# Optimization experiments

Measured on AMD Instinct MI355X. Metric: run time of the kernel, lower is better.

Reference implementation:

```python
import jax, jax.numpy as jnp
import numpy as np

N_NODES = 20000
OUT_DEG = 16
E = N_NODES * OUT_DEG          # 320000 directed edges
F = 20                          # edge_features
H3 = 3 * F


def _lin(key, fan_in, fan_out):
    kw, kb = jax.random.split(key)
    bound = 1.0 / np.sqrt(fan_in)
    W = jax.random.uniform(kw, (fan_in, fan_out), jnp.float32, -bound, bound)
    b = jax.random.uniform(kb, (fan_out,), jnp.float32, -bound, bound)
    return W, b


def setup_inputs() -> dict:
    key = jax.random.key(0)
    rng = np.random.default_rng(0)
    # graph: every node has exactly OUT_DEG out-edges, no self-loops
    src = np.repeat(np.arange(N_NODES, dtype=np.int64), OUT_DEG)
    dst = (src + 1 + rng.integers(0, N_NODES - 1, size=E)) % N_NODES
    edge_index = jnp.asarray(np.stack([src, dst]), dtype=jnp.int32)
    # edge adjacency per _build_edge_adj: edge i=(u->v) pairs with each out-edge j of v.
    # Edges are grouped by src, so out-edges of node v are [v*OUT_DEG, v*OUT_DEG+OUT_DEG).
    # No self-loops => i != j always, so exactly E*OUT_DEG pairs.
    adj_src = jnp.asarray(np.repeat(np.arange(E, dtype=np.int64), OUT_DEG).astype(np.int32))
    adj_nbr = jnp.asarray((dst[:, None] * OUT_DEG + np.arange(OUT_DEG)).reshape(-1).astype(np.int32))

    ks = jax.random.split(key, 8)
    edge_attr = jax.random.normal(ks[0], (E, F), jnp.float32)
    msg_W1, msg_b1 = _lin(ks[1], 2 * F, 32)
    msg_W2, msg_b2 = _lin(ks[2], 32, F)
    # torch GRUCell params: weight_ih/hh are [3H, H]
    bound = 1.0 / np.sqrt(F)
    g = jax.random.split(ks[3], 4)
    gru_Wih = jax.random.uniform(g[0], (H3, F), jnp.float32, -bound, bound)
    gru_Whh = jax.random.uniform(g[1], (H3, F), jnp.float32, -bound, bound)
    gru_bih = jax.random.uniform(g[2], (H3,), jnp.float32, -bound, bound)
    gru_bhh = jax.random.uniform(g[3], (H3,), jnp.float32, -bound, bound)
    ro_W1, ro_b1 = _lin(ks[4], F, 64)
    ro_W2, ro_b2 = _lin(ks[5], 64, 32)
    ro_W3, ro_b3 = _lin(ks[6], 32, 1)
    return {
        'edge_attr': edge_attr,
        'msg_W1': msg_W1, 'msg_b1': msg_b1, 'msg_W2': msg_W2, 'msg_b2': msg_b2,
        'gru_Wih': gru_Wih, 'gru_Whh': gru_Whh, 'gru_bih': gru_bih, 'gru_bhh': gru_bhh,
        'ro_W1': ro_W1, 'ro_b1': ro_b1, 'ro_W2': ro_W2, 'ro_b2': ro_b2,
        'ro_W3': ro_W3, 'ro_b3': ro_b3,
        'edge_index': edge_index, 'adj_src': adj_src, 'adj_nbr': adj_nbr,
    }


def reference(edge_attr, msg_W1, msg_b1, msg_W2, msg_b2,
              gru_Wih, gru_Whh, gru_bih, gru_bhh,
              ro_W1, ro_b1, ro_W2, ro_b2, ro_W3, ro_b3,
              edge_index, adj_src, adj_nbr):
    num_e = edge_attr.shape[0]

    def step(h, _):
        h_i = h[adj_src]                       # [P, F] gather
        h_j = h[adj_nbr]                       # [P, F] gather
        m = jnp.concatenate([h_i, h_j], axis=-1)  # [P, 2F]
        m = jax.nn.selu(m @ msg_W1 + msg_b1) @ msg_W2 + msg_b2  # [P, F]
        agg = jax.ops.segment_sum(m, adj_src, num_segments=num_e)  # scatter_add
        # torch.nn.GRUCell(agg, h)
        gi = agg @ gru_Wih.T + gru_bih
        gh = h @ gru_Whh.T + gru_bhh
        i_r, i_z, i_n = jnp.split(gi, 3, axis=-1)
        h_r, h_z, h_n = jnp.split(gh, 3, axis=-1)
        r = jax.nn.sigmoid(i_r + h_r)
        z = jax.nn.sigmoid(i_z + h_z)
        n = jnp.tanh(i_n + r * h_n)
        return (1.0 - z) * n + z * h, None

    h_t, _ = jax.lax.scan(step, edge_attr, None, length=4)
    h_base = h_t[:num_e]  # num_edges == E here
    x = jax.nn.selu(h_base @ ro_W1 + ro_b1)
    x = jax.nn.selu(x @ ro_W2 + ro_b2)
    w = jax.nn.softplus(x @ ro_W3 + ro_b3).squeeze(-1) + 0.1
    return jnp.clip(w, 0.1, 10.0)
```

## Files before the change

### kernel.cpp

```cpp
#include <hip/hip_runtime.h>
#include <hip/hip_fp16.h>

#define E_EDGES 320000
#define NF 20

typedef float v4 __attribute__((ext_vector_type(4)));
typedef float v2f __attribute__((ext_vector_type(2)));

#if defined(__has_builtin)
# if __has_builtin(__builtin_elementwise_fma)
#  define EWFMA(a,b,c) __builtin_elementwise_fma((a),(b),(c))
# endif
#endif
#ifndef EWFMA
# define EWFMA(a,b,c) ((a)*(b)+(c))
#endif
#if defined(__has_builtin)
# if __has_builtin(__builtin_elementwise_max)
#  define EWMAX(a,b) __builtin_elementwise_max((a),(b))
#  define EWMIN(a,b) __builtin_elementwise_min((a),(b))
# endif
#endif

#if defined(__has_builtin)
# if __has_builtin(__builtin_amdgcn_exp2f)
#  define EX2F(x) __builtin_amdgcn_exp2f(x)
# endif
#endif
#ifndef EX2F
# define EX2F(x) exp2f(x)
#endif

#define LOG2E_F 1.4426950408889634f
#define SELU_SCALE 1.0507009873554805f
#define SELU_ALPHA 1.6732632423543772f
#define SELU_KA (SELU_SCALE * SELU_ALPHA)
#define SELU_SC2 (SELU_SCALE / LOG2E_F)

__device__ __forceinline__ v4 bc4(float s) { return (v4){s, s, s, s}; }
__device__ __forceinline__ v4 v4z() { return (v4){0.f, 0.f, 0.f, 0.f}; }

#define DPP_XOR1 0xB1
#define DPP_XOR2 0x4E
template<int CTRL>
__device__ __forceinline__ float dppf(float x) {
    return __builtin_bit_cast(float,
        __builtin_amdgcn_update_dpp(0, __builtin_bit_cast(int, x), CTRL, 0xF, 0xF, true));
}
template<int CTRL>
__device__ __forceinline__ v4 dpp4(v4 x) {
    v4 r;
    r.x = dppf<CTRL>(x.x); r.y = dppf<CTRL>(x.y);
    r.z = dppf<CTRL>(x.z); r.w = dppf<CTRL>(x.w);
    return r;
}

__device__ __forceinline__ float selu_f(float x) {
    const float scale = SELU_SCALE;
    const float alpha = SELU_ALPHA;
    float p = fmaxf(x, 0.f);
    float m = fminf(x, 0.f);
    float e = __expf(m);
    return fmaf(scale, p, scale * alpha * (e - 1.f));
}
__device__ __forceinline__ float sigmoid_f(float x) {
    return 1.f / (1.f + __expf(-x));
}
__device__ __forceinline__ v4 selu4(v4 x) {
    const float scale = SELU_SCALE;
    const float ka = SELU_KA;
#ifdef EWMAX
    v4 p = EWMAX(x, v4z());
    v4 m = EWMIN(x, v4z());
#else
    v4 p = {fmaxf(x.x,0.f), fmaxf(x.y,0.f), fmaxf(x.z,0.f), fmaxf(x.w,0.f)};
    v4 m = {fminf(x.x,0.f), fminf(x.y,0.f), fminf(x.z,0.f), fminf(x.w,0.f)};
#endif
    v4 e = {__expf(m.x), __expf(m.y), __expf(m.z), __expf(m.w)};
    return EWFMA(bc4(scale), p, EWFMA(bc4(ka), e, bc4(-ka)));
}

__device__ __forceinline__ float hsum4(v4 x) {
    v2f lo = __builtin_shufflevector(x, x, 0, 1);
    v2f hi = __builtin_shufflevector(x, x, 2, 3);
    v2f h = lo + hi;
    return h.x + h.y;
}

__device__ __forceinline__ float dot20v(v4 a0, v4 a1, v4 a2, v4 a3, v4 a4,
                                        const v4* __restrict__ w) {
    v4 w0 = w[0], w1 = w[1], w2 = w[2], w3 = w[3], w4 = w[4];
    v4 x = a0 * w0;
    x = EWFMA(a1, w1, x); x = EWFMA(a2, w2, x);
    x = EWFMA(a3, w3, x); x = EWFMA(a4, w4, x);
    return hsum4(x);
}
__device__ __forceinline__ void dot20_dualv(const v4* __restrict__ w,
    v4 a0, v4 a1, v4 a2, v4 a3, v4 a4,
    v4 b0, v4 b1, v4 b2, v4 b3, v4 b4,
    float& r0, float& r1)
{
    v4 w0 = w[0], w1 = w[1], w2 = w[2], w3 = w[3], w4 = w[4];
    v4 xa = a0 * w0;
    xa = EWFMA(a1, w1, xa); xa = EWFMA(a2, w2, xa);
    xa = EWFMA(a3, w3, xa); xa = EWFMA(a4, w4, xa);
    v4 xb = b0 * w0;
    xb = EWFMA(b1, w1, xb); xb = EWFMA(b2, w2, xb);
    xb = EWFMA(b3, w3, xb); xb = EWFMA(b4, w4, xb);
    r0 = hsum4(xa);
    r1 = hsum4(xb);
}
__device__ __forceinline__ void h8_to_v4x2(uint4 r, v4& lo, v4& hi) {
    float2 fa = __half22float2(__builtin_bit_cast(__half2, r.x));
    float2 fb = __half22float2(__builtin_bit_cast(__half2, r.y));
    float2 fc = __half22float2(__builtin_bit_cast(__half2, r.z));
    float2 fd = __half22float2(__builtin_bit_cast(__half2, r.w));
    lo = (v4){fa.x, fa.y, fb.x, fb.y};
    hi = (v4){fc.x, fc.y, fd.x, fd.y};
}
__device__ __forceinline__ uint4 f8_to_h8(v4 lo, v4 hi) {
    uint4 r;
    r.x = __builtin_bit_cast(unsigned, __floats2half2_rn(lo.x, lo.y));
    r.y = __builtin_bit_cast(unsigned, __floats2half2_rn(lo.z, lo.w));
    r.z = __builtin_bit_cast(unsigned, __floats2half2_rn(hi.x, hi.y));
    r.w = __builtin_bit_cast(unsigned, __floats2half2_rn(hi.z, hi.w));
    return r;
}

#define FOR20(X) \
  X(0, v0.x) X(1, v0.y) X(2, v0.z) X(3, v0.w) \
  X(4, v1.x) X(5, v1.y) X(6, v1.z) X(7, v1.w) \
  X(8, v2.x) X(9, v2.y) X(10, v2.z) X(11, v2.w) \
  X(12, v3.x) X(13, v3.y) X(14, v3.z) X(15, v3.w) \
  X(16, v4v.x) X(17, v4v.y) X(18, v4v.z) X(19, v4v.w)

#define FOR20_2(X) \
  X(0, va0.x, vb0.x) X(1, va0.y, vb0.y) X(2, va0.z, vb0.z) X(3, va0.w, vb0.w) \
  X(4, va1.x, vb1.x) X(5, va1.y, vb1.y) X(6, va1.z, vb1.z) X(7, va1.w, vb1.w) \
  X(8, va2.x, vb2.x) X(9, va2.y, vb2.y) X(10, va2.z, vb2.z) X(11, va2.w, vb2.w) \
  X(12, va3.x, vb3.x) X(13, va3.y, vb3.y) X(14, va3.z, vb3.z) X(15, va3.w, vb3.w) \
  X(16, va4.x, vb4.x) X(17, va4.y, vb4.y) X(18, va4.z, vb4.z) X(19, va4.w, vb4.w)

#define FOR8S2(X) \
  X(0, sa0.x, sb0.x) X(1, sa0.y, sb0.y) X(2, sa0.z, sb0.z) X(3, sa0.w, sb0.w) \
  X(4, sa1.x, sb1.x) X(5, sa1.y, sb1.y) X(6, sa1.z, sb1.z) X(7, sa1.w, sb1.w)

__global__ void __launch_bounds__(256) kernel_B0(
    const float* __restrict__ h, const float* __restrict__ W1,
    const float* __restrict__ b1, __half* __restrict__ B)
{
    __shared__ __align__(16) float sw[640];
    __shared__ __align__(16) float sbias[32];
    for (int i = threadIdx.x; i < 640; i += 256) sw[i] = W1[640 + i] * LOG2E_F;
    if (threadIdx.x < 32) sbias[threadIdx.x] = b1[threadIdx.x] * LOG2E_F;
    __syncthreads();
    int e = blockIdx.x * 256 + threadIdx.x;
    const v4* hp = reinterpret_cast<const v4*>(h + (size_t)e * NF);
    v4 v0 = hp[0], v1 = hp[1], v2 = hp[2], v3 = hp[3], v4v = hp[4];
    const v4* bi = reinterpret_cast<const v4*>(sbias);
    v4 c0 = bi[0], c1 = bi[1], c2 = bi[2], c3 = bi[3],
       c4 = bi[4], c5 = bi[5], c6 = bi[6], c7 = bi[7];
    #define BSTEP(f, hf) { v4 t_ = bc4(hf); const v4* w_ = (const v4*)&sw[(f)*32]; \
        c0 = EWFMA(t_, w_[0], c0); c1 = EWFMA(t_, w_[1], c1); \
        c2 = EWFMA(t_, w_[2], c2); c3 = EWFMA(t_, w_[3], c3); \
        c4 = EWFMA(t_, w_[4], c4); c5 = EWFMA(t_, w_[5], c5); \
        c6 = EWFMA(t_, w_[6], c6); c7 = EWFMA(t_, w_[7], c7); }
    FOR20(BSTEP)
    #undef BSTEP
    uint4* Bp = reinterpret_cast<uint4*>(B + (size_t)e * 32);
    Bp[0] = f8_to_h8(c0, c1); Bp[1] = f8_to_h8(c2, c3);
    Bp[2] = f8_to_h8(c4, c5); Bp[3] = f8_to_h8(c6, c7);
}

template<bool WRITEB>
__global__ void __launch_bounds__(256) kernel_stepT(
    const float* __restrict__ h_in, float* __restrict__ h_out,
    const __half* __restrict__ Br, const int* __restrict__ dst,
    const float* __restrict__ W1, const float* __restrict__ b1,
    const float* __restrict__ W2, const float* __restrict__ b2,
    const float* __restrict__ Wih, const float* __restrict__ Whh,
    const float* __restrict__ bih, const float* __restrict__ bhh,
    __half* __restrict__ Bw)
{
    __shared__ __align__(16) float sW1[640];
    __shared__ __align__(16) float sW1h[640];
    __shared__ __align__(16) float sb1h[32];
    __shared__ __align__(16) float sW2[640];
    __shared__ __align__(16) float sb2v[20];
    __shared__ __align__(16) float sCorr[20];
    __shared__ __align__(16) float sWih[1200];
    __shared__ __align__(16) float sWhh[1200];
    __shared__ float sbih[60];
    __shared__ float sbhh[60];
    for (int i = threadIdx.x; i < 640; i += 256) {
        sW1[i] = W1[i] * LOG2E_F;
        sW2[i] = W2[i];
        if (WRITEB) sW1h[i] = W1[640 + i] * LOG2E_F;
    }
    for (int i = threadIdx.x; i < 1200; i += 256) { sWih[i] = Wih[i]; sWhh[i] = Whh[i]; }
    if (threadIdx.x < 20) sb2v[threadIdx.x] = b2[threadIdx.x];
    else if (threadIdx.x >= 64 && threadIdx.x < 124) sbih[threadIdx.x - 64] = bih[threadIdx.x - 64];
    else if (threadIdx.x >= 128 && threadIdx.x < 188) sbhh[threadIdx.x - 128] = bhh[threadIdx.x - 128];
    else if (WRITEB && threadIdx.x >= 192 && threadIdx.x < 224)
        sb1h[threadIdx.x - 192] = b1[threadIdx.x - 192] * LOG2E_F;
    __syncthreads();
    if (threadIdx.x < 20) {
        float s = 0.f;
        #pragma unroll
        for (int o = 0; o < 32; o++) s += sW2[o * 20 + threadIdx.x];
        sCorr[threadIdx.x] = 16.f * (sb2v[threadIdx.x] - SELU_KA * s);
    }
    __syncthreads();

    int t = blockIdx.x * 256 + threadIdx.x;
    int p = t >> 2;
    int q = t & 3;
    int ob = q * 8;
    int e0 = p * 2, e1 = p * 2 + 1;

    int2 dd = *reinterpret_cast<const int2*>(dst + e0);
    int d0 = dd.x, d1 = dd.y;

    const v4* hp0 = reinterpret_cast<const v4*>(h_in + (size_t)e0 * NF);
    const v4* hp1 = reinterpret_cast<const v4*>(h_in + (size_t)e1 * NF);
    v4 va0 = hp0[0], va1 = hp0[1], va2 = hp0[2], va3 = hp0[3], va4 = hp0[4];
    v4 vb0 = hp1[0], vb1 = hp1[1], vb2 = hp1[2], vb3 = hp1[3], vb4 = hp1[4];

    v4 aa0 = v4z(), aa1 = v4z(), ab0 = v4z(), ab1 = v4z();
    #define ASTEP2(f, h0, h1) { const v4* w_ = (const v4*)&sW1[(f)*32 + ob]; \
        v4 w0_ = w_[0], w1_ = w_[1]; \
        v4 t0_ = bc4(h0), t1_ = bc4(h1); \
        aa0 = EWFMA(t0_, w0_, aa0); aa1 = EWFMA(t0_, w1_, aa1); \
        ab0 = EWFMA(t1_, w0_, ab0); ab1 = EWFMA(t1_, w1_, ab1); }
    FOR20_2(ASTEP2)
    #undef ASTEP2

    const uint4* Bp0 = reinterpret_cast<const uint4*>(Br) + (size_t)d0 * 64 + q;
    const uint4* Bp1 = reinterpret_cast<const uint4*>(Br) + (size_t)d1 * 64 + q;
    v4 sa0 = v4z(), sa1 = v4z(), sb0 = v4z(), sb1 = v4z();
    {
        v4 kav = bc4(SELU_KA), scv = bc4(SELU_SC2), z4 = v4z();
        #define SELUACC(s_, a_, b_) { v4 x_ = (a_) + (b_); \
            v4 p_ = EWMAX(x_, z4); v4 m_ = EWMIN(x_, z4); \
            v4 e_ = {EX2F(m_.x), EX2F(m_.y), EX2F(m_.z), EX2F(m_.w)}; \
            s_ = EWFMA(kav, e_, s_); s_ = EWFMA(scv, p_, s_); }
        #pragma unroll 4
        for (int k = 0; k < 16; k++) {
            uint4 rA = Bp0[k * 4];
            uint4 rB = Bp1[k * 4];
            v4 loA, hiA, loB, hiB;
            h8_to_v4x2(rA, loA, hiA);
            h8_to_v4x2(rB, loB, hiB);
            SELUACC(sa0, aa0, loA);
            SELUACC(sa1, aa1, hiA);
            SELUACC(sb0, ab0, loB);
            SELUACC(sb1, ab1, hiB);
        }
        #undef SELUACC
    }

    v4 ga0 = v4z(), ga1 = v4z(), ga2 = v4z(), ga3 = v4z(), ga4 = v4z();
    v4 gb0 = v4z(), gb1 = v4z(), gb2 = v4z(), gb3 = v4z(), gb4 = v4z();
    #define AGGS2(j, c0_, c1_) { const v4* w_ = (const v4*)&sW2[(ob + (j)) * 20]; \
        v4 w0_ = w_[0], w1_ = w_[1], w2_ = w_[2], w3_ = w_[3], w4_ = w_[4]; \
        v4 u_ = bc4(c0_), vv_ = bc4(c1_); \
        ga0 = EWFMA(u_, w0_, ga0); ga1 = EWFMA(u_, w1_, ga1); ga2 = EWFMA(u_, w2_, ga2); \
        ga3 = EWFMA(u_, w3_, ga3); ga4 = EWFMA(u_, w4_, ga4); \
        gb0 = EWFMA(vv_, w0_, gb0); gb1 = EWFMA(vv_, w1_, gb1); gb2 = EWFMA(vv_, w2_, gb2); \
        gb3 = EWFMA(vv_, w3_, gb3); gb4 = EWFMA(vv_, w4_, gb4); }
    FOR8S2(AGGS2)
    #undef AGGS2

    #define BFLY(CTRL) { \
        ga0 = ga0 + dpp4<CTRL>(ga0); ga1 = ga1 + dpp4<CTRL>(ga1); \
        ga2 = ga2 + dpp4<CTRL>(ga2); ga3 = ga3 + dpp4<CTRL>(ga3); \
        ga4 = ga4 + dpp4<CTRL>(ga4); \
        gb0 = gb0 + dpp4<CTRL>(gb0); gb1 = gb1 + dpp4<CTRL>(gb1); \
        gb2 = gb2 + dpp4<CTRL>(gb2); gb3 = gb3 + dpp4<CTRL>(gb3); \
        gb4 = gb4 + dpp4<CTRL>(gb4); }
    BFLY(DPP_XOR1)
    BFLY(DPP_XOR2)
    #undef BFLY

    {
        const v4* cp = reinterpret_cast<const v4*>(sCorr);
        v4 c0 = cp[0], c1 = cp[1], c2 = cp[2], c3 = cp[3], c4 = cp[4];
        ga0 = ga0 + c0; ga1 = ga1 + c1; ga2 = ga2 + c2; ga3 = ga3 + c3; ga4 = ga4 + c4;
        gb0 = gb0 + c0; gb1 = gb1 + c1; gb2 = gb2 + c2; gb3 = gb3 + c3; gb4 = gb4 + c4;
    }

    v4 ba0, ba1, bb0, bb1;
    if (WRITEB) {
        const v4* b1p = reinterpret_cast<const v4*>(&sb1h[ob]);
        ba0 = b1p[0]; ba1 = b1p[1];
        bb0 = b1p[0]; bb1 = b1p[1];
    }

    for (int i = 0; i < 5; i++) {
        int c = q * 5 + i;
        float ir0, ir1, iz0, iz1, in0, in1, hr0, hr1, hz0, hz1, hn0, hn1;
        dot20_dualv((const v4*)&sWih[c * 20],        ga0, ga1, ga2, ga3, ga4,
                    gb0, gb1, gb2, gb3, gb4, ir0, ir1);
        dot20_dualv((const v4*)&sWih[(20 + c) * 20], ga0, ga1, ga2, ga3, ga4,
                    gb0, gb1, gb2, gb3, gb4, iz0, iz1);
        dot20_dualv((const v4*)&sWih[(40 + c) * 20], ga0, ga1, ga2, ga3, ga4,
                    gb0, gb1, gb2, gb3, gb4, in0, in1);
        dot20_dualv((const v4*)&sWhh[c * 20],        va0, va1, va2, va3, va4,
                    vb0, vb1, vb2, vb3, vb4, hr0, hr1);
        dot20_dualv((const v4*)&sWhh[(20 + c) * 20], va0, va1, va2, va3, va4,
                    vb0, vb1, vb2, vb3, vb4, hz0, hz1);
        dot20_dualv((const v4*)&sWhh[(40 + c) * 20], va0, va1, va2, va3, va4,
                    vb0, vb1, vb2, vb3, vb4, hn0, hn1);
        float bi_r = sbih[c], bi_z = sbih[20 + c], bi_n = sbih[40 + c];
        float bh_r = sbhh[c], bh_z = sbhh[20 + c], bh_n = sbhh[40 + c];
        float nh0, nh1;
        {
            float r = sigmoid_f(bi_r + ir0 + bh_r + hr0);
            float z = sigmoid_f(bi_z + iz0 + bh_z + hz0);
            float xn = bi_n + in0 + r * (bh_n + hn0);
            xn = fminf(fmaxf(xn, -20.f), 20.f);
            float tt = __expf(2.f * xn);
            float n = (tt - 1.f) / (tt + 1.f);
            float hc = h_in[(size_t)e0 * NF + c];
            nh0 = (1.f - z) * n + z * hc;
            h_out[(size_t)e0 * NF + c] = nh0;
        }
        {
            float r = sigmoid_f(bi_r + ir1 + bh_r + hr1);
            float z = sigmoid_f(bi_z + iz1 + bh_z + hz1);
            float xn = bi_n + in1 + r * (bh_n + hn1);
            xn = fminf(fmaxf(xn, -20.f), 20.f);
            float tt = __expf(2.f * xn);
            float n = (tt - 1.f) / (tt + 1.f);
            float hc = h_in[(size_t)e1 * NF + c];
            nh1 = (1.f - z) * n + z * hc;
            h_out[(size_t)e1 * NF + c] = nh1;
        }
        if (WRITEB) {
            #define WB1(qq) { \
                float f0_ = dppf<(qq)*0x55>(nh0); \
                float f1_ = dppf<(qq)*0x55>(nh1); \
                const v4* wp_ = reinterpret_cast<const v4*>(&sW1h[((qq)*5 + i) * 32 + ob]); \
                v4 w0_ = wp_[0], w1_ = wp_[1]; \
                v4 t0_ = bc4(f0_), t1_ = bc4(f1_); \
                ba0 = EWFMA(t0_, w0_, ba0); ba1 = EWFMA(t0_, w1_, ba1); \
                bb0 = EWFMA(t1_, w0_, bb0); bb1 = EWFMA(t1_, w1_, bb1); }
            WB1(0) WB1(1) WB1(2) WB1(3)
            #undef WB1
        }
    }
    if (WRITEB) {
        uint4* Bo = reinterpret_cast<uint4*>(Bw);
        Bo[(size_t)e0 * 4 + q] = f8_to_h8(ba0, ba1);
        Bo[(size_t)e1 * 4 + q] = f8_to_h8(bb0, bb1);
    }
}

__global__ void __launch_bounds__(256) kernel_readout(
    const float* __restrict__ h,
    const float* __restrict__ W1, const float* __restrict__ b1,
    const float* __restrict__ W2, const float* __restrict__ b2,
    const float* __restrict__ W3, const float* __restrict__ b3,
    float* __restrict__ out)
{
    __shared__ __align__(16) float sW1t[1280];
    __shared__ float sb1[64];
    __shared__ __align__(16) float sW2[2048];
    __shared__ __align__(16) float sb2v[32];
    __shared__ __align__(16) float sW3[32];
    __shared__ float sb3;
    for (int i = threadIdx.x; i < 1280; i += 256) {
        int f = i >> 6, o = i & 63;
        sW1t[o * 20 + f] = W1[i];
    }
    for (int i = threadIdx.x; i < 2048; i += 256) sW2[i] = W2[i];
    if (threadIdx.x < 64) sb1[threadIdx.x] = b1[threadIdx.x];
    else if (threadIdx.x >= 64 && threadIdx.x < 96) sb2v[threadIdx.x - 64] = b2[threadIdx.x - 64];
    else if (threadIdx.x >= 96 && threadIdx.x < 128) sW3[threadIdx.x - 96] = W3[threadIdx.x - 96];
    if (threadIdx.x == 128) sb3 = b3[0];
    __syncthreads();

    int e = blockIdx.x * 256 + threadIdx.x;
    const v4* hp = reinterpret_cast<const v4*>(h + (size_t)e * NF);
    v4 v0 = hp[0], v1 = hp[1], v2 = hp[2], v3 = hp[3], v4v = hp[4];

    const v4* b2p = reinterpret_cast<const v4*>(sb2v);
    v4 x20 = b2p[0], x21 = b2p[1], x22 = b2p[2], x23 = b2p[3],
       x24 = b2p[4], x25 = b2p[5], x26 = b2p[6], x27 = b2p[7];
    for (int o = 0; o < 64; o++) {
        float x1 = sb1[o] + dot20v(v0, v1, v2, v3, v4v, (const v4*)&sW1t[o * 20]);
        x1 = selu_f(x1);
        v4 xb = bc4(x1);
        const v4* w = (const v4*)&sW2[o * 32];
        x20 = EWFMA(xb, w[0], x20); x21 = EWFMA(xb, w[1], x21);
        x22 = EWFMA(xb, w[2], x22); x23 = EWFMA(xb, w[3], x23);
        x24 = EWFMA(xb, w[4], x24); x25 = EWFMA(xb, w[5], x25);
        x26 = EWFMA(xb, w[6], x26); x27 = EWFMA(xb, w[7], x27);
    }
    const v4* w3p = reinterpret_cast<const v4*>(sW3);
    v4 accv = selu4(x20) * w3p[0];
    accv = EWFMA(selu4(x21), w3p[1], accv);
    accv = EWFMA(selu4(x22), w3p[2], accv);
    accv = EWFMA(selu4(x23), w3p[3], accv);
    accv = EWFMA(selu4(x24), w3p[4], accv);
    accv = EWFMA(selu4(x25), w3p[5], accv);
    accv = EWFMA(selu4(x26), w3p[6], accv);
    accv = EWFMA(selu4(x27), w3p[7], accv);
    float acc = sb3 + hsum4(accv);
    float sp = fmaxf(acc, 0.f) + log1pf(__expf(-fabsf(acc)));
    float w = sp + 0.1f;
    w = fminf(fmaxf(w, 0.1f), 10.f);
    out[e] = w;
}

extern "C" void kernel_launch(void* const* d_in, const int* in_sizes, int n_in,
                              void* d_out, int out_size, void* d_ws, size_t ws_size,
                              hipStream_t stream) {
    const float* edge_attr = (const float*)d_in[0];
    const float* msg_W1   = (const float*)d_in[1];
    const float* msg_b1   = (const float*)d_in[2];
    const float* msg_W2   = (const float*)d_in[3];
    const float* msg_b2   = (const float*)d_in[4];
    const float* gru_Wih  = (const float*)d_in[5];
    const float* gru_Whh  = (const float*)d_in[6];
    const float* gru_bih  = (const float*)d_in[7];
    const float* gru_bhh  = (const float*)d_in[8];
    const float* ro_W1    = (const float*)d_in[9];
    const float* ro_b1    = (const float*)d_in[10];
    const float* ro_W2    = (const float*)d_in[11];
    const float* ro_b2    = (const float*)d_in[12];
    const float* ro_W3    = (const float*)d_in[13];
    const float* ro_b3    = (const float*)d_in[14];
    const int* edge_index = (const int*)d_in[15];
    const int* dst = edge_index + E_EDGES;

    float*  h_ws = (float*)d_ws;
    __half* BtA  = (__half*)(h_ws + (size_t)E_EDGES * NF);
    __half* BtB  = BtA + (size_t)E_EDGES * 32;

    size_t need = (size_t)E_EDGES * NF * sizeof(float)
                + 2 * (size_t)E_EDGES * 32 * sizeof(__half);
    bool fused = ws_size >= need;

    dim3 block(256);
    dim3 gridB(E_EDGES / 256);
    dim3 gridS(E_EDGES * 2 / 256);

    kernel_B0<<<gridB, block, 0, stream>>>(edge_attr, msg_W1, msg_b1, BtA);

    const float* hin = edge_attr;
    __half* Bin = BtA;
    __half* Bout = BtB;
    for (int s = 0; s < 4; s++) {
        if (!fused && s > 0)
            kernel_B0<<<gridB, block, 0, stream>>>(hin, msg_W1, msg_b1, BtA);
        if (fused && s < 3) {
            kernel_stepT<true><<<gridS, block, 0, stream>>>(hin, h_ws, Bin, dst,
                msg_W1, msg_b1, msg_W2, msg_b2, gru_Wih, gru_Whh, gru_bih, gru_bhh,
                Bout);
            __half* tmp = Bin; Bin = Bout; Bout = tmp;
        } else {
            kernel_stepT<false><<<gridS, block, 0, stream>>>(hin, h_ws, Bin, dst,
                msg_W1, msg_b1, msg_W2, msg_b2, gru_Wih, gru_Whh, gru_bih, gru_bhh,
                nullptr);
        }
        hin = h_ws;
    }
    kernel_readout<<<gridB, block, 0, stream>>>(h_ws, ro_W1, ro_b1, ro_W2, ro_b2,
                                                ro_W3, ro_b3, (float*)d_out);
}
```

Measured before the change: 522.0 us.

## Split readout MLP across thread pairs with DPP reduction and exp2-folded SELU

Rewrites the readout kernel so each edge is handled by two adjacent threads. Each thread computes half of the 64 hidden units as an outer-product accumulation. The partial layer-2 sums are combined with a DPP xor-1 swap. Weights and biases are pre-scaled by log2(e) at shared-memory load so the SELU can use exp2 directly. This doubles thread count and halves per-thread serial work and register pressure, at the cost of redundant input loads, a duplicate layer-3 computation, and a predicated store.

```diff
diff --git a/kernel.cpp b/kernel.cpp
--- a/kernel.cpp
+++ b/kernel.cpp
@@ -55,20 +55,10 @@
     return r;
 }
 
-__device__ __forceinline__ float selu_f(float x) {
-    const float scale = SELU_SCALE;
-    const float alpha = SELU_ALPHA;
-    float p = fmaxf(x, 0.f);
-    float m = fminf(x, 0.f);
-    float e = __expf(m);
-    return fmaf(scale, p, scale * alpha * (e - 1.f));
-}
 __device__ __forceinline__ float sigmoid_f(float x) {
     return 1.f / (1.f + __expf(-x));
 }
-__device__ __forceinline__ v4 selu4(v4 x) {
-    const float scale = SELU_SCALE;
-    const float ka = SELU_KA;
+__device__ __forceinline__ v4 selu4p(v4 x) {
 #ifdef EWMAX
     v4 p = EWMAX(x, v4z());
     v4 m = EWMIN(x, v4z());
@@ -76,8 +66,8 @@
     v4 p = {fmaxf(x.x,0.f), fmaxf(x.y,0.f), fmaxf(x.z,0.f), fmaxf(x.w,0.f)};
     v4 m = {fminf(x.x,0.f), fminf(x.y,0.f), fminf(x.z,0.f), fminf(x.w,0.f)};
 #endif
-    v4 e = {__expf(m.x), __expf(m.y), __expf(m.z), __expf(m.w)};
-    return EWFMA(bc4(scale), p, EWFMA(bc4(ka), e, bc4(-ka)));
+    v4 e = {EX2F(m.x), EX2F(m.y), EX2F(m.z), EX2F(m.w)};
+    return EWFMA(bc4(SELU_SC2), p, EWFMA(bc4(SELU_KA), e, bc4(-SELU_KA)));
 }
 
 __device__ __forceinline__ float hsum4(v4 x) {
@@ -87,14 +77,6 @@
     return h.x + h.y;
 }
 
-__device__ __forceinline__ float dot20v(v4 a0, v4 a1, v4 a2, v4 a3, v4 a4,
-                                        const v4* __restrict__ w) {
-    v4 w0 = w[0], w1 = w[1], w2 = w[2], w3 = w[3], w4 = w[4];
-    v4 x = a0 * w0;
-    x = EWFMA(a1, w1, x); x = EWFMA(a2, w2, x);
-    x = EWFMA(a3, w3, x); x = EWFMA(a4, w4, x);
-    return hsum4(x);
-}
 __device__ __forceinline__ void dot20_dualv(const v4* __restrict__ w,
     v4 a0, v4 a1, v4 a2, v4 a3, v4 a4,
     v4 b0, v4 b1, v4 b2, v4 b3, v4 b4,
@@ -356,61 +338,92 @@
     }
 }
 
-__global__ void __launch_bounds__(256) kernel_readout(
+__global__ void __launch_bounds__(256) kernel_readout2(
     const float* __restrict__ h,
     const float* __restrict__ W1, const float* __restrict__ b1,
     const float* __restrict__ W2, const float* __restrict__ b2,
     const float* __restrict__ W3, const float* __restrict__ b3,
     float* __restrict__ out)
 {
-    __shared__ __align__(16) float sW1t[1280];
-    __shared__ float sb1[64];
+    __shared__ __align__(16) float sW1[1280];
+    __shared__ __align__(16) float sb1[64];
     __shared__ __align__(16) float sW2[2048];
-    __shared__ __align__(16) float sb2v[32];
+    __shared__ __align__(16) float sb2[32];
     __shared__ __align__(16) float sW3[32];
     __shared__ float sb3;
-    for (int i = threadIdx.x; i < 1280; i += 256) {
-        int f = i >> 6, o = i & 63;
-        sW1t[o * 20 + f] = W1[i];
-    }
-    for (int i = threadIdx.x; i < 2048; i += 256) sW2[i] = W2[i];
-    if (threadIdx.x < 64) sb1[threadIdx.x] = b1[threadIdx.x];
-    else if (threadIdx.x >= 64 && threadIdx.x < 96) sb2v[threadIdx.x - 64] = b2[threadIdx.x - 64];
-    else if (threadIdx.x >= 96 && threadIdx.x < 128) sW3[threadIdx.x - 96] = W3[threadIdx.x - 96];
-    if (threadIdx.x == 128) sb3 = b3[0];
+    for (int i = threadIdx.x; i < 1280; i += 256) sW1[i] = W1[i] * LOG2E_F;
+    for (int i = threadIdx.x; i < 2048; i += 256) sW2[i] = W2[i] * LOG2E_F;
+    {
+        int tx = threadIdx.x;
+        if (tx < 64) sb1[tx] = b1[tx] * LOG2E_F;
+        else if (tx < 96) sb2[tx - 64] = b2[tx - 64] * LOG2E_F;
+        else if (tx < 128) sW3[tx - 96] = W3[tx - 96];
+        else if (tx == 128) sb3 = b3[0];
+    }
     __syncthreads();
 
-    int e = blockIdx.x * 256 + threadIdx.x;
+    int tid = blockIdx.x * 256 + threadIdx.x;
+    int e = tid >> 1;
+    int half = threadIdx.x & 1;
+    int ob32 = half * 32;
+
     const v4* hp = reinterpret_cast<const v4*>(h + (size_t)e * NF);
     v4 v0 = hp[0], v1 = hp[1], v2 = hp[2], v3 = hp[3], v4v = hp[4];
 
-    const v4* b2p = reinterpret_cast<const v4*>(sb2v);
-    v4 x20 = b2p[0], x21 = b2p[1], x22 = b2p[2], x23 = b2p[3],
-       x24 = b2p[4], x25 = b2p[5], x26 = b2p[6], x27 = b2p[7];
-    for (int o = 0; o < 64; o++) {
-        float x1 = sb1[o] + dot20v(v0, v1, v2, v3, v4v, (const v4*)&sW1t[o * 20]);
-        x1 = selu_f(x1);
-        v4 xb = bc4(x1);
-        const v4* w = (const v4*)&sW2[o * 32];
-        x20 = EWFMA(xb, w[0], x20); x21 = EWFMA(xb, w[1], x21);
-        x22 = EWFMA(xb, w[2], x22); x23 = EWFMA(xb, w[3], x23);
-        x24 = EWFMA(xb, w[4], x24); x25 = EWFMA(xb, w[5], x25);
-        x26 = EWFMA(xb, w[6], x26); x27 = EWFMA(xb, w[7], x27);
-    }
+    const v4* b1p = reinterpret_cast<const v4*>(&sb1[ob32]);
+    v4 a0 = b1p[0], a1 = b1p[1], a2 = b1p[2], a3 = b1p[3],
+       a4 = b1p[4], a5 = b1p[5], a6 = b1p[6], a7 = b1p[7];
+    #define L1S(f, hf) { v4 t_ = bc4(hf); const v4* w_ = (const v4*)&sW1[(f)*64 + ob32]; \
+        a0 = EWFMA(t_, w_[0], a0); a1 = EWFMA(t_, w_[1], a1); \
+        a2 = EWFMA(t_, w_[2], a2); a3 = EWFMA(t_, w_[3], a3); \
+        a4 = EWFMA(t_, w_[4], a4); a5 = EWFMA(t_, w_[5], a5); \
+        a6 = EWFMA(t_, w_[6], a6); a7 = EWFMA(t_, w_[7], a7); }
+    FOR20(L1S)
+    #undef L1S
+    a0 = selu4p(a0); a1 = selu4p(a1); a2 = selu4p(a2); a3 = selu4p(a3);
+    a4 = selu4p(a4); a5 = selu4p(a5); a6 = selu4p(a6); a7 = selu4p(a7);
+
+    v4 y0, y1, y2, y3, y4, y5, y6, y7;
+    if (half == 0) {
+        const v4* b2p = reinterpret_cast<const v4*>(sb2);
+        y0 = b2p[0]; y1 = b2p[1]; y2 = b2p[2]; y3 = b2p[3];
+        y4 = b2p[4]; y5 = b2p[5]; y6 = b2p[6]; y7 = b2p[7];
+    } else {
+        y0 = v4z(); y1 = v4z(); y2 = v4z(); y3 = v4z();
+        y4 = v4z(); y5 = v4z(); y6 = v4z(); y7 = v4z();
+    }
+    #define L2S(s_, ol) { const v4* w_ = (const v4*)&sW2[(size_t)(ob32 + (ol)) * 32]; \
+        v4 t_ = bc4(s_); \
+        y0 = EWFMA(t_, w_[0], y0); y1 = EWFMA(t_, w_[1], y1); \
+        y2 = EWFMA(t_, w_[2], y2); y3 = EWFMA(t_, w_[3], y3); \
+        y4 = EWFMA(t_, w_[4], y4); y5 = EWFMA(t_, w_[5], y5); \
+        y6 = EWFMA(t_, w_[6], y6); y7 = EWFMA(t_, w_[7], y7); }
+    #define S2V(jj, xv) L2S(xv.x, (jj)*4+0) L2S(xv.y, (jj)*4+1) \
+                        L2S(xv.z, (jj)*4+2) L2S(xv.w, (jj)*4+3)
+    S2V(0, a0) S2V(1, a1) S2V(2, a2) S2V(3, a3)
+    S2V(4, a4) S2V(5, a5) S2V(6, a6) S2V(7, a7)
+    #undef S2V
+    #undef L2S
+
+    y0 = y0 + dpp4<DPP_XOR1>(y0); y1 = y1 + dpp4<DPP_XOR1>(y1);
+    y2 = y2 + dpp4<DPP_XOR1>(y2); y3 = y3 + dpp4<DPP_XOR1>(y3);
+    y4 = y4 + dpp4<DPP_XOR1>(y4); y5 = y5 + dpp4<DPP_XOR1>(y5);
+    y6 = y6 + dpp4<DPP_XOR1>(y6); y7 = y7 + dpp4<DPP_XOR1>(y7);
+
     const v4* w3p = reinterpret_cast<const v4*>(sW3);
-    v4 accv = selu4(x20) * w3p[0];
-    accv = EWFMA(selu4(x21), w3p[1], accv);
-    accv = EWFMA(selu4(x22), w3p[2], accv);
-    accv = EWFMA(selu4(x23), w3p[3], accv);
-    accv = EWFMA(selu4(x24), w3p[4], accv);
-    accv = EWFMA(selu4(x25), w3p[5], accv);
-    accv = EWFMA(selu4(x26), w3p[6], accv);
-    accv = EWFMA(selu4(x27), w3p[7], accv);
+    v4 accv = selu4p(y0) * w3p[0];
+    accv = EWFMA(selu4p(y1), w3p[1], accv);
+    accv = EWFMA(selu4p(y2), w3p[2], accv);
+    accv = EWFMA(selu4p(y3), w3p[3], accv);
+    accv = EWFMA(selu4p(y4), w3p[4], accv);
+    accv = EWFMA(selu4p(y5), w3p[5], accv);
+    accv = EWFMA(selu4p(y6), w3p[6], accv);
+    accv = EWFMA(selu4p(y7), w3p[7], accv);
     float acc = sb3 + hsum4(accv);
     float sp = fmaxf(acc, 0.f) + log1pf(__expf(-fabsf(acc)));
     float w = sp + 0.1f;
     w = fminf(fmaxf(w, 0.1f), 10.f);
-    out[e] = w;
+    if (half == 0) out[e] = w;
 }
 
 extern "C" void kernel_launch(void* const* d_in, const int* in_sizes, int n_in,
@@ -466,6 +479,6 @@
         }
         hin = h_ws;
     }
-    kernel_readout<<<gridB, block, 0, stream>>>(h_ws, ro_W1, ro_b1, ro_W2, ro_b2,
-                                                ro_W3, ro_b3, (float*)d_out);
-}
+    kernel_readout2<<<gridS, block, 0, stream>>>(h_ws, ro_W1, ro_b1, ro_W2, ro_b2,
+                                                 ro_W3, ro_b3, (float*)d_out);
+}
```

After: 796.9 us. 52.7% more time.
